# Performance work log

Measured on AMD Instinct MI355X. Metric: run time of the kernel, lower is better.

## Reference

```python
import jax, jax.numpy as jnp
import numpy as np

B, T, I, H, C, L, N_AHEAD = 64, 512, 64, 512, 512, 2, 24


def _lstm_layer(x, w_ih, w_hh, b_ih, b_hh):
    """PyTorch-convention LSTM layer. x: [B,T,in]. Returns (outputs [B,T,H], hT, cT)."""
    bsz = x.shape[0]
    hdim = w_hh.shape[1]
    bias = b_ih + b_hh

    def step(carry, xt):
        h, c = carry
        g = xt @ w_ih.T + h @ w_hh.T + bias  # [B, 4H], gate order i,f,g,o
        i, f, gg, o = jnp.split(g, 4, axis=-1)
        c = jax.nn.sigmoid(f) * c + jax.nn.sigmoid(i) * jnp.tanh(gg)
        h = jax.nn.sigmoid(o) * jnp.tanh(c)
        return (h, c), h

    init = (jnp.zeros((bsz, hdim), x.dtype), jnp.zeros((bsz, hdim), x.dtype))
    (hT, cT), hs = jax.lax.scan(step, init, jnp.swapaxes(x, 0, 1))
    return jnp.swapaxes(hs, 0, 1), hT, cT


def setup_inputs() -> dict:
    key = jax.random.key(0)
    ks = jax.random.split(key, 16)
    s = 0.04  # ~ 1/sqrt(H) init scale
    d = {
        "x": jax.random.normal(ks[0], (B, T, I), jnp.float32),
        "w_ih0": jax.random.normal(ks[1], (4 * H, I), jnp.float32) * s,
        "w_hh0": jax.random.normal(ks[2], (4 * H, H), jnp.float32) * s,
        "b_ih0": jax.random.normal(ks[3], (4 * H,), jnp.float32) * s,
        "b_hh0": jax.random.normal(ks[4], (4 * H,), jnp.float32) * s,
        "w_ih1": jax.random.normal(ks[5], (4 * H, H), jnp.float32) * s,
        "w_hh1": jax.random.normal(ks[6], (4 * H, H), jnp.float32) * s,
        "b_ih1": jax.random.normal(ks[7], (4 * H,), jnp.float32) * s,
        "b_hh1": jax.random.normal(ks[8], (4 * H,), jnp.float32) * s,
        "w_ih_dec": jax.random.normal(ks[9], (4 * H, C), jnp.float32) * s,
        "w_hh_dec": jax.random.normal(ks[10], (4 * H, H), jnp.float32) * s,
        "b_ih_dec": jax.random.normal(ks[11], (4 * H,), jnp.float32) * s,
        "b_hh_dec": jax.random.normal(ks[12], (4 * H,), jnp.float32) * s,
        "w_fc": jax.random.normal(ks[13], (C, H), jnp.float32) * s,
        "b_fc": jax.random.normal(ks[14], (C,), jnp.float32) * s,
    }
    return d


def reference(x, w_ih0, w_hh0, b_ih0, b_hh0, w_ih1, w_hh1, b_ih1, b_hh1,
              w_ih_dec, w_hh_dec, b_ih_dec, b_hh_dec, w_fc, b_fc):
    # ---- encoder: 2-layer LSTM, batch_first ----
    h0_out, _, _ = _lstm_layer(x, w_ih0, w_hh0, b_ih0, b_hh0)
    enc, hT, cT = _lstm_layer(h0_out, w_ih1, w_hh1, b_ih1, b_hh1)  # enc: [B,T,H]

    bsz = x.shape[0]
    dec_bias = b_ih_dec + b_hh_dec
    dec_in0 = jnp.zeros((bsz, C), x.dtype)

    def dec_step(carry, _):
        h, c, dec_in = carry
        aw = jax.nn.softmax(jnp.einsum('bth,bh->bt', enc, h), axis=1)  # [B,T]
        ctx = jnp.einsum('bt,bth->bh', aw, enc)                         # [B,H]
        xi = dec_in + ctx                                               # requires C == H
        g = xi @ w_ih_dec.T + h @ w_hh_dec.T + dec_bias
        i, f, gg, o = jnp.split(g, 4, axis=-1)
        c = jax.nn.sigmoid(f) * c + jax.nn.sigmoid(i) * jnp.tanh(gg)
        h = jax.nn.sigmoid(o) * jnp.tanh(c)
        pred = h @ w_fc.T + b_fc                                        # [B,C]
        return (h, c, pred), pred

    _, preds = jax.lax.scan(dec_step, (hT, cT, dec_in0), None, length=N_AHEAD)
    return jnp.swapaxes(preds, 0, 1)  # [B, n_ahead, C]
```

## Files before the change

### kernel.cpp

```cpp
#include <hip/hip_runtime.h>

#define BATCH  64
#define TT     512
#define IDIM   64
#define HDIM   512
#define NAHEAD 24
#define HB     (HDIM * BATCH)

#define WIH0_OFF   0
#define WHH0_OFF   512
#define WIH1_OFF   4608
#define WHH1_OFF   8704
#define SCR_OFF    12800
#define GL_OFF     30208
#define BIAS_OFF   31232
#define ENC_SMEM_FLOATS 31248
#define ENC_SMEM_BYTES  (ENC_SMEM_FLOATS * 4)

__device__ __forceinline__ float4 ld4(const float* p) {
  return *reinterpret_cast<const float4*>(p);
}
__device__ __forceinline__ float sigm(float x) { return 1.0f / (1.0f + expf(-x)); }

__device__ __forceinline__ void flag_barrier(unsigned* flags, unsigned* release,
                                             unsigned epoch, int bid) {
  asm volatile("s_waitcnt vmcnt(0)" ::: "memory");
  __syncthreads();
  if (threadIdx.x == 0)
    __hip_atomic_store(&flags[(size_t)bid * 16], epoch,
                       __ATOMIC_RELAXED, __HIP_MEMORY_SCOPE_AGENT);
  asm volatile("" ::: "memory");
  if (bid == 0 && threadIdx.x < 64) {
    const int l = threadIdx.x;
    for (;;) {
      bool ok = true;
#pragma unroll
      for (int i = 0; i < 4; ++i) {
        unsigned v = __hip_atomic_load(&flags[(size_t)(l * 4 + i) * 16],
                                       __ATOMIC_RELAXED, __HIP_MEMORY_SCOPE_AGENT);
        ok &= (v >= epoch);
      }
      if (__all(ok)) break;
      __builtin_amdgcn_s_sleep(1);
    }
    if (threadIdx.x == 0)
      __hip_atomic_store(release, epoch, __ATOMIC_RELAXED,
                         __HIP_MEMORY_SCOPE_AGENT);
  }
  if (threadIdx.x == 0) {
    while (__hip_atomic_load(release, __ATOMIC_RELAXED,
                             __HIP_MEMORY_SCOPE_AGENT) < epoch)
      __builtin_amdgcn_s_sleep(1);
  }
  __syncthreads();
  asm volatile("" ::: "memory");
}

#define STAGE8(dst, base)                                     \
  _Pragma("unroll") for (int i = 0; i < 8; ++i) dst[i] = (base)[i * BATCH];

#define BURN8(sv_, ev_, J)                                                    \
  do {                                                                        \
    if (t < TT) {                                                             \
      _Pragma("unroll") for (int c = 0; c < 8; c += 4) {                      \
        _Pragma("unroll") for (int d = 0; d < 8; ++d) {                       \
          float4 w = ld4(&smem[WHH0_OFF + d * HDIM + ks * 32 + (J) * 8 + c]); \
          a0[d] += sv_[c]*w.x + sv_[c+1]*w.y + sv_[c+2]*w.z + sv_[c+3]*w.w;   \
        }                                                                     \
      }                                                                       \
    }                                                                         \
    if (t >= 1) {                                                             \
      _Pragma("unroll") for (int c = 0; c < 8; c += 4) {                      \
        _Pragma("unroll") for (int d = 0; d < 8; ++d) {                       \
          float4 w = ld4(&smem[WIH1_OFF + d * HDIM + ks * 32 + (J) * 8 + c]); \
          a1[d] += sv_[c]*w.x + sv_[c+1]*w.y + sv_[c+2]*w.z + sv_[c+3]*w.w;   \
        }                                                                     \
        _Pragma("unroll") for (int d = 0; d < 8; ++d) {                       \
          float4 w = ld4(&smem[WHH1_OFF + d * HDIM + ks * 32 + (J) * 8 + c]); \
          a1[d] += ev_[c]*w.x + ev_[c+1]*w.y + ev_[c+2]*w.z + ev_[c+3]*w.w;   \
        }                                                                     \
      }                                                                       \
    }                                                                         \
  } while (0)

__global__ __launch_bounds__(1024, 4)
void encoder_coop(const float* __restrict__ xT,
                  const float* __restrict__ w_ih0, const float* __restrict__ w_hh0,
                  const float* __restrict__ b_ih0, const float* __restrict__ b_hh0,
                  const float* __restrict__ w_ih1, const float* __restrict__ w_hh1,
                  const float* __restrict__ b_ih1, const float* __restrict__ b_hh1,
                  float* __restrict__ seq0,
                  float* __restrict__ enc,
                  float* __restrict__ cst1,
                  unsigned* flags, unsigned* release)
{
  extern __shared__ float smem[];
  const int tid = threadIdx.x;
  const int bid = blockIdx.x;
  const int j0  = bid * 2;
  const int b   = tid & 63;
  const int ks  = tid >> 6;

  for (int idx = tid; idx < 8 * IDIM; idx += 1024) {
    int d = idx >> 6, k = idx & 63;
    size_t r = (size_t)((d >> 1) * HDIM + j0 + (d & 1));
    smem[WIH0_OFF + idx] = w_ih0[r * IDIM + k];
  }
  for (int idx = tid; idx < 8 * HDIM; idx += 1024) {
    int d = idx >> 9, k = idx & 511;
    size_t r = (size_t)((d >> 1) * HDIM + j0 + (d & 1));
    smem[WHH0_OFF + idx] = w_hh0[r * HDIM + k];
    smem[WIH1_OFF + idx] = w_ih1[r * HDIM + k];
    smem[WHH1_OFF + idx] = w_hh1[r * HDIM + k];
  }
  if (tid < 16) {
    int d = tid & 7;
    size_t r = (size_t)((d >> 1) * HDIM + j0 + (d & 1));
    smem[BIAS_OFF + tid] = (tid < 8) ? (b_ih0[r] + b_hh0[r])
                                     : (b_ih1[r] + b_hh1[r]);
  }
  __syncthreads();

  float c0 = 0.f;
  float c1 = 0.f;

  for (int t = 0; t <= TT; ++t) {
    const float* sp = seq0 + (size_t)t * HB + (size_t)(ks * 32) * BATCH + b;
    const float* ep = enc + (size_t)(t >= 1 ? t - 1 : 0) * HB
                          + (size_t)(ks * 32) * BATCH + b;

    float svA[8], svB[8], evA[8], evB[8];
    float xv[4] = {0.f, 0.f, 0.f, 0.f};

    STAGE8(svA, sp);
    if (t >= 1) STAGE8(evA, ep);
    if (t < TT) {
      const float* xp = xT + (size_t)t * IDIM * BATCH
                           + (size_t)(ks * 4) * BATCH + b;
#pragma unroll
      for (int i = 0; i < 4; ++i) xv[i] = xp[i * BATCH];
    }

    float a0[8] = {0.f,0.f,0.f,0.f,0.f,0.f,0.f,0.f};
    float a1[8] = {0.f,0.f,0.f,0.f,0.f,0.f,0.f,0.f};

    STAGE8(svB, sp + 8 * BATCH);
    if (t >= 1) STAGE8(evB, ep + 8 * BATCH);

    if (t < TT) {
#pragma unroll
      for (int d = 0; d < 8; ++d) {
        float4 w = ld4(&smem[WIH0_OFF + d * IDIM + ks * 4]);
        a0[d] += xv[0]*w.x + xv[1]*w.y + xv[2]*w.z + xv[3]*w.w;
      }
    }
    BURN8(svA, evA, 0);

    STAGE8(svA, sp + 16 * BATCH);
    if (t >= 1) STAGE8(evA, ep + 16 * BATCH);
    BURN8(svB, evB, 1);

    STAGE8(svB, sp + 24 * BATCH);
    if (t >= 1) STAGE8(evB, ep + 24 * BATCH);
    BURN8(svA, evA, 2);

    BURN8(svB, evB, 3);

#pragma unroll
    for (int d = 0; d < 8; ++d)
      smem[SCR_OFF + (d * 64 + b) * 17 + ks] = a0[d];
#pragma unroll
    for (int d = 0; d < 8; ++d)
      smem[SCR_OFF + ((8 + d) * 64 + b) * 17 + ks] = a1[d];
    __syncthreads();

    {
      const int dd = tid >> 6, bb = tid & 63;
      float s = 0.f;
#pragma unroll
      for (int i = 0; i < 16; ++i) s += smem[SCR_OFF + (dd * 64 + bb) * 17 + i];
      smem[GL_OFF + dd * 64 + bb] = s + smem[BIAS_OFF + dd];
    }
    __syncthreads();

    if (tid < 256) {
      const int bb = tid & 63, u = tid >> 6;
      if (u < 2) {
        if (t < TT) {
          const int cl = u;
          float gi = smem[GL_OFF + (0 + cl) * 64 + bb];
          float gf = smem[GL_OFF + (2 + cl) * 64 + bb];
          float gg = smem[GL_OFF + (4 + cl) * 64 + bb];
          float go = smem[GL_OFF + (6 + cl) * 64 + bb];
          float cn = sigm(gf) * c0 + sigm(gi) * tanhf(gg);
          float hn = sigm(go) * tanhf(cn);
          c0 = cn;
          __hip_atomic_store(
              &seq0[(size_t)(t + 1) * HB + (size_t)(j0 + cl) * BATCH + bb],
              hn, __ATOMIC_RELAXED, __HIP_MEMORY_SCOPE_AGENT);
        }
      } else {
        if (t >= 1) {
          const int cl = u - 2;
          float gi = smem[GL_OFF + (8 + 0 + cl) * 64 + bb];
          float gf = smem[GL_OFF + (8 + 2 + cl) * 64 + bb];
          float gg = smem[GL_OFF + (8 + 4 + cl) * 64 + bb];
          float go = smem[GL_OFF + (8 + 6 + cl) * 64 + bb];
          float cn = sigm(gf) * c1 + sigm(gi) * tanhf(gg);
          float hn = sigm(go) * tanhf(cn);
          c1 = cn;
          __hip_atomic_store(
              &enc[(size_t)t * HB + (size_t)(j0 + cl) * BATCH + bb],
              hn, __ATOMIC_RELAXED, __HIP_MEMORY_SCOPE_AGENT);
        }
      }
    }

    if (t < TT) flag_barrier(flags, release, (unsigned)(t + 1), bid);
  }

  if (tid >= 128 && tid < 256)
    cst1[(size_t)(j0 + ((tid >> 6) - 2)) * BATCH + (tid & 63)] = c1;
}

template <int DIN0>
__device__ __forceinline__ void cell_tile2(
    int j0, const float* __restrict__ in0,
    const float* __restrict__ h_in,
    const float* __restrict__ w_ih,
    const float* __restrict__ w_hh,
    const float* __restrict__ b_ih, const float* __restrict__ b_hh,
    float* __restrict__ c_state,
    float* __restrict__ h_out,
    float* __restrict__ sm)
{
  const int tid = threadIdx.x;
  const int b  = tid & 63;
  const int ks = tid >> 6;
  constexpr int K  = DIN0 + HDIM;
  constexpr int KS = K / 16;
  const int k0 = ks * KS, k1 = k0 + KS;
  const int a0 = (k0 < DIN0) ? k0 : DIN0;
  const int a1 = (k1 < DIN0) ? k1 : DIN0;
  const int c0 = (k0 > DIN0) ? k0 - DIN0 : 0;
  const int c1 = (k1 > DIN0) ? k1 - DIN0 : 0;

  const float* wi = w_ih + (size_t)j0 * DIN0;
  const float* wh = w_hh + (size_t)j0 * HDIM;

  float acc[8] = {0.f, 0.f, 0.f, 0.f, 0.f, 0.f, 0.f, 0.f};

#pragma unroll 2
  for (int k = a0; k < a1; k += 4) {
    float x0 = in0[(k + 0) * BATCH + b];
    float x1 = in0[(k + 1) * BATCH + b];
    float x2 = in0[(k + 2) * BATCH + b];
    float x3 = in0[(k + 3) * BATCH + b];
#pragma unroll
    for (int d = 0; d < 8; ++d) {
      float4 w = ld4(wi + (size_t)((d >> 1) * HDIM + (d & 1)) * DIN0 + k);
      acc[d] += x0 * w.x + x1 * w.y + x2 * w.z + x3 * w.w;
    }
  }
#pragma unroll 2
  for (int k = c0; k < c1; k += 4) {
    float h0 = h_in[(k + 0) * BATCH + b];
    float h1 = h_in[(k + 1) * BATCH + b];
    float h2 = h_in[(k + 2) * BATCH + b];
    float h3 = h_in[(k + 3) * BATCH + b];
#pragma unroll
    for (int d = 0; d < 8; ++d) {
      float4 w = ld4(wh + (size_t)((d >> 1) * HDIM + (d & 1)) * HDIM + k);
      acc[d] += h0 * w.x + h1 * w.y + h2 * w.z + h3 * w.w;
    }
  }

  float* gl = sm + 8 * 64 * 17;
#pragma unroll
  for (int d = 0; d < 8; ++d) sm[(d * 64 + b) * 17 + ks] = acc[d];
  __syncthreads();

  if (tid < 512) {
    const int dd = tid >> 6, bb = tid & 63;
    float s = 0.f;
#pragma unroll
    for (int i = 0; i < 16; ++i) s += sm[(dd * 64 + bb) * 17 + i];
    const int r = (dd >> 1) * HDIM + j0 + (dd & 1);
    gl[dd * 64 + bb] = s + b_ih[r] + b_hh[r];
  }
  __syncthreads();

  if (tid < 128) {
    const int bb = tid & 63, cl = tid >> 6;
    const int jc = j0 + cl;
    float gi = gl[(0 + cl) * 64 + bb];
    float gf = gl[(2 + cl) * 64 + bb];
    float gg = gl[(4 + cl) * 64 + bb];
    float go = gl[(6 + cl) * 64 + bb];
    float cold = c_state[(size_t)jc * BATCH + bb];
    float cn = sigm(gf) * cold + sigm(gi) * tanhf(gg);
    float hn = sigm(go) * tanhf(cn);
    c_state[(size_t)jc * BATCH + bb] = cn;
    h_out[(size_t)jc * BATCH + bb] = hn;
  }
  __syncthreads();
}

__global__ __launch_bounds__(1024, 1)
void lstm_step(int t,
               const float* __restrict__ xT,
               const float* __restrict__ w_ih0, const float* __restrict__ w_hh0,
               const float* __restrict__ b_ih0, const float* __restrict__ b_hh0,
               const float* __restrict__ w_ih1, const float* __restrict__ w_hh1,
               const float* __restrict__ b_ih1, const float* __restrict__ b_hh1,
               float* __restrict__ seq0, float* __restrict__ enc,
               float* __restrict__ cst0, float* __restrict__ cst1)
{
  __shared__ float sm[8 * 64 * 17 + 8 * 64];
  const int j0 = blockIdx.x * 2;
  if (t < TT)
    cell_tile2<IDIM>(j0, xT + (size_t)t * IDIM * BATCH,
                     seq0 + (size_t)t * HB,
                     w_ih0, w_hh0, b_ih0, b_hh0,
                     cst0, seq0 + (size_t)(t + 1) * HB, sm);
  if (t >= 1)
    cell_tile2<HDIM>(j0, seq0 + (size_t)t * HB,
                     enc + (size_t)(t - 1) * HB,
                     w_ih1, w_hh1, b_ih1, b_hh1,
                     cst1, enc + (size_t)t * HB, sm);
}

__global__ __launch_bounds__(1024, 1)
void dec_gates(const float* __restrict__ xi, const float* __restrict__ h_cur,
               const float* __restrict__ w_ih, const float* __restrict__ w_hh,
               const float* __restrict__ b_ih, const float* __restrict__ b_hh,
               float* __restrict__ cst, float* __restrict__ h_out)
{
  __shared__ float sm[8 * 64 * 17 + 8 * 64];
  cell_tile2<HDIM>(blockIdx.x * 2, xi, h_cur, w_ih, w_hh, b_ih, b_hh,
                   cst, h_out, sm);
}

__global__ __launch_bounds__(512, 2)
void attn_scores(const float* __restrict__ enc,
                 const float* __restrict__ h_cur,
                 float* __restrict__ scores)
{
  __shared__ float red[2][8][64];
  const int tid = threadIdx.x;
  const int b  = tid & 63;
  const int ks = tid >> 6;
  const int t0 = blockIdx.x * 2;
  const float* e0 = enc + (size_t)(t0 + 1) * HB + ks * 64 * BATCH;
  const float* e1 = e0 + HB;
  const float* hr = h_cur + ks * 64 * BATCH;
  float a0 = 0.f, a1 = 0.f;
#pragma unroll 4
  for (int k = 0; k < 64; ++k) {
    float hv = hr[k * BATCH + b];
    a0 += hv * e0[k * BATCH + b];
    a1 += hv * e1[k * BATCH + b];
  }
  red[0][ks][b] = a0;
  red[1][ks][b] = a1;
  __syncthreads();
  if (tid < 128) {
    int tl = tid >> 6;
    float s = 0.f;
#pragma unroll
    for (int i = 0; i < 8; ++i) s += red[tl][i][b];
    scores[(size_t)(t0 + tl) * BATCH + b] = s;
  }
}

__global__ __launch_bounds__(512, 2)
void attn_ctx(const float* __restrict__ enc,
              const float* __restrict__ scores,
              const float* __restrict__ h_cur,
              const float* __restrict__ w_fc, const float* __restrict__ b_fc,
              float* __restrict__ xi,
              float* __restrict__ out,
              int s)
{
  __shared__ float red[8][2][64];
  __shared__ float mz[2][64];
  __shared__ float ctxv[2][64];
  const int tid = threadIdx.x;
  const int b  = tid & 63;
  const int ts = tid >> 6;
  const int hc0 = blockIdx.x * 2;

  float m = -1e30f;
  for (int t = ts * 64; t < ts * 64 + 64; ++t)
    m = fmaxf(m, scores[(size_t)t * BATCH + b]);
  red[ts][0][b] = m;
  __syncthreads();
  if (tid < 64) {
    float mm = red[0][0][b];
#pragma unroll
    for (int i = 1; i < 8; ++i) mm = fmaxf(mm, red[i][0][b]);
    mz[0][b] = mm;
  }
  __syncthreads();
  m = mz[0][b];
  float z = 0.f;
  for (int t = ts * 64; t < ts * 64 + 64; ++t)
    z += expf(scores[(size_t)t * BATCH + b] - m);
  red[ts][1][b] = z;
  __syncthreads();
  if (tid < 64) {
    float zz = 0.f;
#pragma unroll
    for (int i = 0; i < 8; ++i) zz += red[i][1][b];
    mz[1][b] = 1.f / zz;
  }
  __syncthreads();
  const float rZ = mz[1][b];

  float a0 = 0.f, a1 = 0.f;
  const float* eb = enc + HB + (size_t)hc0 * BATCH + b;
  for (int t = ts * 64; t < ts * 64 + 64; ++t) {
    float p = expf(scores[(size_t)t * BATCH + b] - m) * rZ;
    a0 += p * eb[(size_t)t * HB];
    a1 += p * eb[(size_t)t * HB + BATCH];
  }
  __syncthreads();
  red[ts][0][b] = a0;
  red[ts][1][b] = a1;
  __syncthreads();
  if (tid < 128) {
    int cl = tid >> 6;
    float c = 0.f;
#pragma unroll
    for (int i = 0; i < 8; ++i) c += red[i][cl][b];
    ctxv[cl][b] = c;
  }

  float p0 = 0.f, p1 = 0.f;
  if (s >= 1) {
    const float* w0 = w_fc + (size_t)hc0 * HDIM + ts * 64;
    const float* w1 = w0 + HDIM;
    const float* hr = h_cur + ts * 64 * BATCH;
#pragma unroll 2
    for (int k = 0; k < 64; k += 4) {
      float4 wa = ld4(w0 + k), wb = ld4(w1 + k);
      float h0 = hr[(k + 0) * BATCH + b], h1 = hr[(k + 1) * BATCH + b];
      float h2 = hr[(k + 2) * BATCH + b], h3 = hr[(k + 3) * BATCH + b];
      p0 += wa.x * h0 + wa.y * h1 + wa.z * h2 + wa.w * h3;
      p1 += wb.x * h0 + wb.y * h1 + wb.z * h2 + wb.w * h3;
    }
  }
  __syncthreads();
  red[ts][0][b] = p0;
  red[ts][1][b] = p1;
  __syncthreads();
  if (tid < 128) {
    int cl = tid >> 6;
    int cc = hc0 + cl;
    float pred = 0.f;
    if (s >= 1) {
#pragma unroll
      for (int i = 0; i < 8; ++i) pred += red[i][cl][b];
      pred += b_fc[cc];
      out[((size_t)b * NAHEAD + (s - 1)) * HDIM + cc] = pred;
    }
    xi[(size_t)cc * BATCH + b] = ctxv[cl][b] + pred;
  }
}

__global__ __launch_bounds__(512, 2)
void fc_out(const float* __restrict__ h, const float* __restrict__ w_fc,
            const float* __restrict__ b_fc, float* __restrict__ out, int srow)
{
  __shared__ float red[8][2][64];
  const int tid = threadIdx.x;
  const int b  = tid & 63;
  const int ks = tid >> 6;
  const int cc0 = blockIdx.x * 2;
  const float* w0 = w_fc + (size_t)cc0 * HDIM + ks * 64;
  const float* w1 = w0 + HDIM;
  const float* hr = h + ks * 64 * BATCH;
  float p0 = 0.f, p1 = 0.f;
#pragma unroll 2
  for (int k = 0; k < 64; k += 4) {
    float4 wa = ld4(w0 + k), wb = ld4(w1 + k);
    float h0 = hr[(k + 0) * BATCH + b], h1 = hr[(k + 1) * BATCH + b];
    float h2 = hr[(k + 2) * BATCH + b], h3 = hr[(k + 3) * BATCH + b];
    p0 += wa.x * h0 + wa.y * h1 + wa.z * h2 + wa.w * h3;
    p1 += wb.x * h0 + wb.y * h1 + wb.z * h2 + wb.w * h3;
  }
  red[ks][0][b] = p0;
  red[ks][1][b] = p1;
  __syncthreads();
  if (tid < 128) {
    int cl = tid >> 6;
    int cc = cc0 + cl;
    float p = 0.f;
#pragma unroll
    for (int i = 0; i < 8; ++i) p += red[i][cl][b];
    out[((size_t)b * NAHEAD + srow) * HDIM + cc] = p + b_fc[cc];
  }
}

__global__ __launch_bounds__(256)
void transpose_x(const float* __restrict__ x, float* __restrict__ xT)
{
  __shared__ float tile[64][65];
  const int t = blockIdx.x;
  const int lane = threadIdx.x & 63;
  const int w    = threadIdx.x >> 6;
#pragma unroll
  for (int ii = 0; ii < 16; ++ii) {
    int b = w * 16 + ii;
    tile[b][lane] = x[((size_t)b * TT + t) * IDIM + lane];
  }
  __syncthreads();
#pragma unroll
  for (int ii = 0; ii < 16; ++ii) {
    int i = w * 16 + ii;
    xT[((size_t)t * IDIM + i) * BATCH + lane] = tile[lane][i];
  }
}

extern "C" void kernel_launch(void* const* d_in, const int* in_sizes, int n_in,
                              void* d_out, int out_size, void* d_ws, size_t ws_size,
                              hipStream_t stream) {
  const float* x     = (const float*)d_in[0];
  const float* w_ih0 = (const float*)d_in[1];
  const float* w_hh0 = (const float*)d_in[2];
  const float* b_ih0 = (const float*)d_in[3];
  const float* b_hh0 = (const float*)d_in[4];
  const float* w_ih1 = (const float*)d_in[5];
  const float* w_hh1 = (const float*)d_in[6];
  const float* b_ih1 = (const float*)d_in[7];
  const float* b_hh1 = (const float*)d_in[8];
  const float* w_ihd = (const float*)d_in[9];
  const float* w_hhd = (const float*)d_in[10];
  const float* b_ihd = (const float*)d_in[11];
  const float* b_hhd = (const float*)d_in[12];
  const float* w_fc  = (const float*)d_in[13];
  const float* b_fc  = (const float*)d_in[14];
  float* out = (float*)d_out;

  char* ws = (char*)d_ws;
  size_t off = 0;
  auto alloc = [&](size_t bytes) -> void* {
    void* p = ws + off;
    off += (bytes + 255) & ~(size_t)255;
    return p;
  };

  float* cst0 = (float*)alloc((size_t)HB * 4);
  float* cst1 = (float*)alloc((size_t)HB * 4);
  float* seq0 = (float*)alloc((size_t)(TT + 1) * HB * 4);
  float* enc  = (float*)alloc((size_t)(TT + 1) * HB * 4);
  float* xT   = (float*)alloc((size_t)TT * IDIM * BATCH * 4);
  float* scores = (float*)alloc((size_t)TT * BATCH * 4);
  float* xi     = (float*)alloc((size_t)HB * 4);
  float* hdec   = (float*)alloc((size_t)2 * HB * 4);
  unsigned* flags   = (unsigned*)alloc(256 * 16 * 4);
  unsigned* release = (unsigned*)alloc(256);
  (void)ws_size; (void)in_sizes; (void)n_in; (void)out_size;

  hipMemsetAsync(cst0, 0, (size_t)HB * 4 * 2, stream);
  hipMemsetAsync(seq0, 0, (size_t)HB * 4, stream);
  hipMemsetAsync(enc,  0, (size_t)HB * 4, stream);
  hipMemsetAsync(flags, 0, 256 * 16 * 4, stream);
  hipMemsetAsync(release, 0, 256, stream);

  transpose_x<<<TT, 256, 0, stream>>>(x, xT);

  static bool attr_set = false;
  if (!attr_set) {
    hipFuncSetAttribute(reinterpret_cast<const void*>(encoder_coop),
                        hipFuncAttributeMaxDynamicSharedMemorySize,
                        ENC_SMEM_BYTES);
    attr_set = true;
  }
  void* args[] = {
    (void*)&xT,
    (void*)&w_ih0, (void*)&w_hh0, (void*)&b_ih0, (void*)&b_hh0,
    (void*)&w_ih1, (void*)&w_hh1, (void*)&b_ih1, (void*)&b_hh1,
    (void*)&seq0, (void*)&enc, (void*)&cst1, (void*)&flags, (void*)&release
  };
  hipError_t cerr = hipLaunchCooperativeKernel(
      reinterpret_cast<void*>(encoder_coop), dim3(256), dim3(1024),
      args, (unsigned)ENC_SMEM_BYTES, stream);
  if (cerr != hipSuccess) {
    for (int t = 0; t <= TT; ++t) {
      lstm_step<<<256, 1024, 0, stream>>>(
          t, xT, w_ih0, w_hh0, b_ih0, b_hh0,
          w_ih1, w_hh1, b_ih1, b_hh1, seq0, enc, cst0, cst1);
    }
  }

  const float* h_cur = enc + (size_t)TT * HB;
  for (int s = 0; s < NAHEAD; ++s) {
    attn_scores<<<256, 512, 0, stream>>>(enc, h_cur, scores);
    attn_ctx<<<256, 512, 0, stream>>>(enc, scores, h_cur, w_fc, b_fc,
                                      xi, out, s);
    float* h_nxt = hdec + (size_t)(s & 1) * HB;
    dec_gates<<<256, 1024, 0, stream>>>(xi, h_cur, w_ihd, w_hhd,
                                        b_ihd, b_hhd, cst1, h_nxt);
    h_cur = h_nxt;
  }
  fc_out<<<256, 512, 0, stream>>>(h_cur, w_fc, b_fc, out, NAHEAD - 1);
}
```

Before: 8.993 ms.

## Process two batch elements per thread with packed float2 math in encoder step

Each thread now handles two batch columns (b and b+32) over a 16-wide K slice instead of one batch column over a 32-wide slice. Every shared-memory weight float4 load is therefore reused for two batch elements, and the packed float2 arithmetic can map onto packed FMA instructions. The two half-wave partial sums are combined with a cross-lane shuffle before the shared-memory reduction. In exchange the code adds shuffles, changes the global load pattern to two strided loads per element, and shortens the staging pipeline.

```diff
diff --git a/kernel.cpp b/kernel.cpp
--- a/kernel.cpp
+++ b/kernel.cpp
@@ -17,6 +17,8 @@
 #define ENC_SMEM_FLOATS 31248
 #define ENC_SMEM_BYTES  (ENC_SMEM_FLOATS * 4)
 
+typedef float v2f __attribute__((ext_vector_type(2)));
+
 __device__ __forceinline__ float4 ld4(const float* p) {
   return *reinterpret_cast<const float4*>(p);
 }
@@ -56,28 +58,37 @@
   asm volatile("" ::: "memory");
 }
 
-#define STAGE8(dst, base)                                     \
-  _Pragma("unroll") for (int i = 0; i < 8; ++i) dst[i] = (base)[i * BATCH];
-
-#define BURN8(sv_, ev_, J)                                                    \
+#define STG8(dst, base, off0)                                          \
+  _Pragma("unroll") for (int i = 0; i < 8; ++i) {                      \
+    dst[i].x = (base)[((off0) + i) * BATCH];                           \
+    dst[i].y = (base)[((off0) + i) * BATCH + 32];                      \
+  }
+
+#define BURN_S(sarr, C0)                                                      \
   do {                                                                        \
-    if (t < TT) {                                                             \
-      _Pragma("unroll") for (int c = 0; c < 8; c += 4) {                      \
+    _Pragma("unroll") for (int c = 0; c < 8; c += 4) {                        \
+      if (t < TT) {                                                           \
         _Pragma("unroll") for (int d = 0; d < 8; ++d) {                       \
-          float4 w = ld4(&smem[WHH0_OFF + d * HDIM + ks * 32 + (J) * 8 + c]); \
-          a0[d] += sv_[c]*w.x + sv_[c+1]*w.y + sv_[c+2]*w.z + sv_[c+3]*w.w;   \
+          float4 w = ld4(&smem[WHH0_OFF + d * HDIM + ks * 16 + (C0) + c]);    \
+          a0[d] += sarr[c]*w.x + sarr[c+1]*w.y + sarr[c+2]*w.z + sarr[c+3]*w.w;\
+        }                                                                     \
+      }                                                                       \
+      if (t >= 1) {                                                           \
+        _Pragma("unroll") for (int d = 0; d < 8; ++d) {                       \
+          float4 w = ld4(&smem[WIH1_OFF + d * HDIM + ks * 16 + (C0) + c]);    \
+          a1[d] += sarr[c]*w.x + sarr[c+1]*w.y + sarr[c+2]*w.z + sarr[c+3]*w.w;\
         }                                                                     \
       }                                                                       \
     }                                                                         \
+  } while (0)
+
+#define BURN_E(earr, C0)                                                      \
+  do {                                                                        \
     if (t >= 1) {                                                             \
       _Pragma("unroll") for (int c = 0; c < 8; c += 4) {                      \
         _Pragma("unroll") for (int d = 0; d < 8; ++d) {                       \
-          float4 w = ld4(&smem[WIH1_OFF + d * HDIM + ks * 32 + (J) * 8 + c]); \
-          a1[d] += sv_[c]*w.x + sv_[c+1]*w.y + sv_[c+2]*w.z + sv_[c+3]*w.w;   \
-        }                                                                     \
-        _Pragma("unroll") for (int d = 0; d < 8; ++d) {                       \
-          float4 w = ld4(&smem[WHH1_OFF + d * HDIM + ks * 32 + (J) * 8 + c]); \
-          a1[d] += ev_[c]*w.x + ev_[c+1]*w.y + ev_[c+2]*w.z + ev_[c+3]*w.w;   \
+          float4 w = ld4(&smem[WHH1_OFF + d * HDIM + ks * 16 + (C0) + c]);    \
+          a1[d] += earr[c]*w.x + earr[c+1]*w.y + earr[c+2]*w.z + earr[c+3]*w.w;\
         }                                                                     \
       }                                                                       \
     }                                                                         \
@@ -95,11 +106,13 @@
                   unsigned* flags, unsigned* release)
 {
   extern __shared__ float smem[];
-  const int tid = threadIdx.x;
-  const int bid = blockIdx.x;
-  const int j0  = bid * 2;
-  const int b   = tid & 63;
-  const int ks  = tid >> 6;
+  const int tid  = threadIdx.x;
+  const int bid  = blockIdx.x;
+  const int j0   = bid * 2;
+  const int lane = tid & 63;
+  const int wv   = tid >> 6;
+  const int bp   = tid & 31;
+  const int ks   = tid >> 5;
 
   for (int idx = tid; idx < 8 * IDIM; idx += 1024) {
     int d = idx >> 6, k = idx & 63;
@@ -125,53 +138,53 @@
   float c1 = 0.f;
 
   for (int t = 0; t <= TT; ++t) {
-    const float* sp = seq0 + (size_t)t * HB + (size_t)(ks * 32) * BATCH + b;
+    const float* sp = seq0 + (size_t)t * HB + (size_t)(ks * 16) * BATCH + bp;
     const float* ep = enc + (size_t)(t >= 1 ? t - 1 : 0) * HB
-                          + (size_t)(ks * 32) * BATCH + b;
-
-    float svA[8], svB[8], evA[8], evB[8];
-    float xv[4] = {0.f, 0.f, 0.f, 0.f};
-
-    STAGE8(svA, sp);
-    if (t >= 1) STAGE8(evA, ep);
-    if (t < TT) {
+                          + (size_t)(ks * 16) * BATCH + bp;
+
+    v2f sA[8], sB[8], eA[8], eB[8];
+    v2f xv[4];
+
+    STG8(sA, sp, 0);
+    STG8(sB, sp, 8);
+    if (t < TT && ks < 16) {
       const float* xp = xT + (size_t)t * IDIM * BATCH
-                           + (size_t)(ks * 4) * BATCH + b;
-#pragma unroll
-      for (int i = 0; i < 4; ++i) xv[i] = xp[i * BATCH];
-    }
-
-    float a0[8] = {0.f,0.f,0.f,0.f,0.f,0.f,0.f,0.f};
-    float a1[8] = {0.f,0.f,0.f,0.f,0.f,0.f,0.f,0.f};
-
-    STAGE8(svB, sp + 8 * BATCH);
-    if (t >= 1) STAGE8(evB, ep + 8 * BATCH);
-
-    if (t < TT) {
+                           + (size_t)(ks * 4) * BATCH + bp;
+#pragma unroll
+      for (int i = 0; i < 4; ++i) {
+        xv[i].x = xp[i * BATCH];
+        xv[i].y = xp[i * BATCH + 32];
+      }
+    }
+
+    v2f a0[8], a1[8];
+#pragma unroll
+    for (int d = 0; d < 8; ++d) { a0[d] = 0.f; a1[d] = 0.f; }
+
+    if (t < TT && ks < 16) {
 #pragma unroll
       for (int d = 0; d < 8; ++d) {
         float4 w = ld4(&smem[WIH0_OFF + d * IDIM + ks * 4]);
         a0[d] += xv[0]*w.x + xv[1]*w.y + xv[2]*w.z + xv[3]*w.w;
       }
     }
-    BURN8(svA, evA, 0);
-
-    STAGE8(svA, sp + 16 * BATCH);
-    if (t >= 1) STAGE8(evA, ep + 16 * BATCH);
-    BURN8(svB, evB, 1);
-
-    STAGE8(svB, sp + 24 * BATCH);
-    if (t >= 1) STAGE8(evB, ep + 24 * BATCH);
-    BURN8(svA, evA, 2);
-
-    BURN8(svB, evB, 3);
-
-#pragma unroll
-    for (int d = 0; d < 8; ++d)
-      smem[SCR_OFF + (d * 64 + b) * 17 + ks] = a0[d];
-#pragma unroll
-    for (int d = 0; d < 8; ++d)
-      smem[SCR_OFF + ((8 + d) * 64 + b) * 17 + ks] = a1[d];
+
+    BURN_S(sA, 0);
+    if (t >= 1) STG8(eA, ep, 0);
+    BURN_S(sB, 8);
+    if (t >= 1) STG8(eB, ep, 8);
+    BURN_E(eA, 0);
+    BURN_E(eB, 8);
+
+#pragma unroll
+    for (int d = 0; d < 8; ++d) {
+      float m0x = a0[d].x + __shfl_xor(a0[d].x, 32);
+      float m0y = a0[d].y + __shfl_xor(a0[d].y, 32);
+      smem[SCR_OFF + (d * 64 + lane) * 17 + wv] = (lane >= 32) ? m0y : m0x;
+      float m1x = a1[d].x + __shfl_xor(a1[d].x, 32);
+      float m1y = a1[d].y + __shfl_xor(a1[d].y, 32);
+      smem[SCR_OFF + ((8 + d) * 64 + lane) * 17 + wv] = (lane >= 32) ? m1y : m1x;
+    }
     __syncthreads();
 
     {
```

New measurement: 7.396 ms. 17.8% less time.
